# Kernel tuning notes

Hardware: AMD Instinct MI355X
Metric: run time of the kernel (lower is better)

Reference implementation:

```python
import jax, jax.numpy as jnp
import numpy as np

IN_C, H1, H2, FC1, NCLS = 16, 32, 64, 128, 10
N_NODES, N_EDGES = 20000, 100000


def _glorot(key, shape):
    fan_in, fan_out = shape[0], shape[-1]
    s = jnp.sqrt(6.0 / (fan_in + fan_out))
    return jax.random.uniform(key, shape, jnp.float32, -s, s)


def setup_inputs() -> dict:
    key = jax.random.key(0)
    ks = jax.random.split(key, 20)
    x = jax.random.normal(ks[0], (N_NODES, IN_C), jnp.float32)
    edge_index = jax.random.randint(ks[1], (2, N_EDGES), 0, N_NODES, jnp.int64)
    edge_attr = jax.random.uniform(ks[2], (N_EDGES, 1), jnp.float32)
    return {
        "x": x,
        "edge_index": edge_index,
        "edge_attr": edge_attr,
        # conv1 edge-MLP: 1 -> 25 -> IN_C*H1
        "w1a": _glorot(ks[3], (1, 25)), "b1a": jnp.zeros((25,), jnp.float32),
        "w1b": _glorot(ks[4], (25, IN_C * H1)), "b1b": jnp.zeros((IN_C * H1,), jnp.float32),
        "wr1": _glorot(ks[5], (IN_C, H1)), "bias1": jnp.zeros((H1,), jnp.float32),
        # conv2 edge-MLP: 1 -> 25 -> H1*H2 (=2048)
        "w2a": _glorot(ks[6], (1, 25)), "b2a": jnp.zeros((25,), jnp.float32),
        "w2b": _glorot(ks[7], (25, H1 * H2)), "b2b": jnp.zeros((H1 * H2,), jnp.float32),
        "wr2": _glorot(ks[8], (H1, H2)), "bias2": jnp.zeros((H2,), jnp.float32),
        # trailing FCs
        "fc1_w": _glorot(ks[9], (H2, FC1)), "fc1_b": jnp.zeros((FC1,), jnp.float32),
        "fc2_w": _glorot(ks[10], (FC1, NCLS)), "fc2_b": jnp.zeros((NCLS,), jnp.float32),
    }


def _nnconv(x, src, tgt, edge_attr, wa, ba, wb, bb, wroot, bias, in_c, out_c):
    # per-edge MLP-generated weight matrix [E, in_c, out_c]
    h = jax.nn.relu(edge_attr @ wa + ba) @ wb + bb
    W = h.reshape(-1, in_c, out_c)
    # gather source feats, per-edge matmul, scatter-max to targets
    msg = jnp.einsum("ei,eio->eo", x[src], W)  # [E, out_c]
    agg = jax.ops.segment_max(msg, tgt, num_segments=x.shape[0])
    agg = jnp.where(jnp.isfinite(agg), agg, 0.0)  # nodes with no in-edges -> 0 (PyG behavior)
    return agg + x @ wroot + bias


def reference(x, edge_index, edge_attr,
              w1a, b1a, w1b, b1b, wr1, bias1,
              w2a, b2a, w2b, b2b, wr2, bias2,
              fc1_w, fc1_b, fc2_w, fc2_b):
    src, tgt = edge_index[0], edge_index[1]
    h = jax.nn.elu(_nnconv(x, src, tgt, edge_attr, w1a, b1a, w1b, b1b, wr1, bias1, IN_C, H1))
    h = jax.nn.elu(_nnconv(h, src, tgt, edge_attr, w2a, b2a, w2b, b2b, wr2, bias2, H1, H2))
    h = jax.nn.elu(h @ fc1_w + fc1_b)
    h = h @ fc2_w + fc2_b
    return jax.nn.log_softmax(h, axis=1)
```

## Files before the change

### kernel.cpp

```cpp
#include <hip/hip_runtime.h>
#include <float.h>
#include <math.h>


#define NCONST 25
#define CH1 32
#define CH2 16
#define PACK_MASK 0x1FFFF

typedef float vf16 __attribute__((ext_vector_type(16)));
typedef float vf32 __attribute__((ext_vector_type(32)));

__device__ __forceinline__ void atomicMaxFloat(float* addr, float val) {
    if (val >= 0.f) atomicMax((int*)addr, __float_as_int(val));
    else            atomicMin((unsigned int*)addr, __float_as_uint(val));
}
__device__ __forceinline__ float readlane_f(float v, int l) {
    return __int_as_float(__builtin_amdgcn_readlane(__float_as_int(v), l));
}

__global__ void fill_kernel(float* agg, int nAgg, int* ords, int nOrd, int* hist, int nH) {
    int i = blockIdx.x * blockDim.x + threadIdx.x;
    int stride = gridDim.x * blockDim.x;
    int total = nAgg + nOrd + nH;
    for (; i < total; i += stride) {
        if (i < nAgg) agg[i] = -FLT_MAX;
        else if (i < nAgg + nOrd) ords[i - nAgg] = -1;
        else hist[i - nAgg - nOrd] = 0;
    }
}

__global__ void assign_hist_kernel(const float* __restrict__ ea,
                                   const float* __restrict__ w1a, const float* __restrict__ b1a,
                                   const float* __restrict__ w2a, const float* __restrict__ b2a,
                                   int E, int* __restrict__ segpack, int* __restrict__ hist) {
    __shared__ float t1[NCONST], t2[NCONST];
    __shared__ int lh[64];
    int tid = threadIdx.x;
    if (tid < NCONST) {
        float w = w1a[tid]; t1[tid] = (w != 0.f) ? (-b1a[tid] / w) : INFINITY;
        float v = w2a[tid]; t2[tid] = (v != 0.f) ? (-b2a[tid] / v) : INFINITY;
    }
    if (tid < 64) lh[tid] = 0;
    __syncthreads();
    int e = blockIdx.x * blockDim.x + tid;
    bool valid = e < E;
    if (valid) {
        float a = ea[e];
        int j1 = 0, j2 = 0;
        for (int k = 0; k < NCONST; ++k) { j1 += (t1[k] < a); j2 += (t2[k] < a); }
        segpack[e] = j1 | (j2 << 8);
        atomicAdd(&lh[j1], 1); atomicAdd(&lh[32 + j2], 1);
    }
    __syncthreads();
    if (tid < 64 && lh[tid]) atomicAdd(&hist[tid], lh[tid]);
}

__global__ void scanpad_kernel(const int* __restrict__ hist, int* __restrict__ cur) {
    __shared__ int h[64];
    int tid = threadIdx.x;
    h[tid] = hist[tid];
    __syncthreads();
    if (tid == 0) {
        int off = 0;
        for (int j = 0; j < 26; ++j) { cur[j] = off; off += ((h[j] + CH1 - 1) / CH1) * CH1; }
    } else if (tid == 1) {
        int off = 0;
        for (int j = 0; j < 26; ++j) { cur[32 + j] = off; off += ((h[32 + j] + CH2 - 1) / CH2) * CH2; }
    }
}

__global__ void scatter_kernel(const int* __restrict__ segpack, int E, int* __restrict__ cur,
                               int* __restrict__ order1, int* __restrict__ order2) {
    __shared__ int lh[64], lb[64];
    int tid = threadIdx.x;
    if (tid < 64) lh[tid] = 0;
    __syncthreads();
    int e = blockIdx.x * blockDim.x + tid;
    bool valid = e < E;
    int j1 = 0, j2 = 0, r1 = 0, r2 = 0;
    if (valid) {
        int p = segpack[e]; j1 = p & 0xFF; j2 = p >> 8;
        r1 = atomicAdd(&lh[j1], 1); r2 = atomicAdd(&lh[32 + j2], 1);
    }
    __syncthreads();
    if (tid < 64 && lh[tid]) lb[tid] = atomicAdd(&cur[tid], lh[tid]);
    __syncthreads();
    if (valid) {
        order1[lb[j1] + r1] = (j1 << 17) | e;
        order2[lb[32 + j2] + r2] = (j2 << 17) | e;
    }
}

__global__ void build_uv_fused(const float* w1a, const float* b1a, const float* w1b, const float* b1b,
                               const float* w2a, const float* b2a, const float* w2b, const float* b2b,
                               float* U1, float* V1, float* U2, float* V2) {
    __shared__ float swa[NCONST], sba[NCONST], st[NCONST];
    __shared__ int sr[NCONST];
    __shared__ unsigned msk_sh;
    int seg = blockIdx.y;
    int bx = blockIdx.x;
    int conv = (bx < 2) ? 0 : 1;
    const float* wa = conv ? w2a : w1a;
    const float* ba = conv ? b2a : b1a;
    int tid = threadIdx.x;
    if (tid < NCONST) {
        float w = wa[tid], b = ba[tid];
        swa[tid] = w; sba[tid] = b;
        st[tid] = (w != 0.f) ? (-b / w) : INFINITY;
    }
    __syncthreads();
    if (tid < NCONST) {
        int rk = 0;
        for (int l = 0; l < NCONST; ++l) rk += (st[l] < st[tid]) ? 1 : 0;
        sr[tid] = rk;
    }
    __syncthreads();
    if (tid == 0) {
        unsigned m = 0;
        for (int k = 0; k < NCONST; ++k) {
            float w = swa[k];
            bool act = (w > 0.f) ? (seg > sr[k])
                     : (w < 0.f) ? (seg <= sr[k])
                                 : (sba[k] > 0.f);
            if (act) m |= (1u << k);
        }
        msk_sh = m;
    }
    __syncthreads();
    unsigned msk = msk_sh;
    if (conv == 0) {
        int idx = bx * 256 + tid;
        float u = 0.f, v = 0.f;
        for (int k = 0; k < NCONST; ++k)
            if (msk & (1u << k)) { float w = w1b[k * 512 + idx]; u = fmaf(swa[k], w, u); v = fmaf(sba[k], w, v); }
        v += b1b[idx];
        U1[seg * 512 + idx] = u; V1[seg * 512 + idx] = v;
    } else {
        int idx = (bx - 2) * 256 + tid;
        float u = 0.f, v = 0.f;
        for (int k = 0; k < NCONST; ++k)
            if (msk & (1u << k)) { float w = w2b[k * 2048 + idx]; u = fmaf(swa[k], w, u); v = fmaf(sba[k], w, v); }
        v += b2b[idx];
        U2[seg * 2048 + idx] = u; V2[seg * 2048 + idx] = v;
    }
}

__global__ void __launch_bounds__(256, 4)
edge1_kernel(const float* __restrict__ xin, const int* __restrict__ src,
             const int* __restrict__ tgt, const float* __restrict__ ea,
             const int* __restrict__ order, int cap,
             const float* __restrict__ U, const float* __restrict__ V,
             float* __restrict__ agg) {
    int wid = (blockIdx.x * blockDim.x + threadIdx.x) >> 6;
    int lane = threadIdx.x & 63;
    int base = wid * CH1;
    if (base >= cap) return;
    int pk = order[base + (lane & (CH1 - 1))];
    int p0 = __builtin_amdgcn_readfirstlane(pk);
    if (p0 < 0) return;
    int seg = p0 >> 17;
    int ev = (pk < 0) ? 0 : (pk & PACK_MASK);
    int sv = src[ev], tv = tgt[ev];
    float av = ea[ev];
    int half = lane >> 5, c = lane & 31;
    vf16 Ur, Vr;
    {
        const float* Us = U + seg * 512 + c;
        const float* Vs = V + seg * 512 + c;
#pragma unroll
        for (int i = 0; i < 16; ++i) { Ur[i] = Us[i * 32]; Vr[i] = Vs[i * 32]; }
    }
#pragma unroll
    for (int t = 0; t < CH1; t += 2) {
        int pA = __builtin_amdgcn_readlane(pk, t);
        int pB = __builtin_amdgcn_readlane(pk, t + 1);
        int sA = __builtin_amdgcn_readlane(sv, t);
        int sB = __builtin_amdgcn_readlane(sv, t + 1);
        int tA = __builtin_amdgcn_readlane(tv, t);
        int tB = __builtin_amdgcn_readlane(tv, t + 1);
        float aA = readlane_f(av, t);
        float aB = readlane_f(av, t + 1);
        const float* xA = xin + sA * 16;
        const float* xB = xin + sB * 16;
        float ah = half ? aB : aA;
        int   th = half ? tB : tA;
        int   ph = half ? pB : pA;
        float acc = 0.f;
#pragma unroll
        for (int i = 0; i < 16; ++i) {
            float xi = half ? xB[i] : xA[i];
            acc = fmaf(xi, fmaf(ah, Ur[i], Vr[i]), acc);
        }
        if (ph >= 0) atomicMaxFloat(&agg[th * 32 + c], acc);
    }
}

__global__ void __launch_bounds__(256, 2)
edge2_kernel(const float* __restrict__ xin, const int* __restrict__ src,
             const int* __restrict__ tgt, const float* __restrict__ ea,
             const int* __restrict__ order, int cap,
             const float* __restrict__ U, const float* __restrict__ V,
             float* __restrict__ agg) {
    int wid = (blockIdx.x * blockDim.x + threadIdx.x) >> 6;
    int lane = threadIdx.x & 63;
    int base = wid * CH2;
    if (base >= cap) return;
    int pk = order[base + (lane & (CH2 - 1))];
    int p0 = __builtin_amdgcn_readfirstlane(pk);
    if (p0 < 0) return;
    int seg = p0 >> 17;
    int ev = (pk < 0) ? 0 : (pk & PACK_MASK);
    int sv = src[ev], tv = tgt[ev];
    float av = ea[ev];
    vf32 Ur, Vr;
    {
        const float* Us = U + seg * 2048 + lane;
        const float* Vs = V + seg * 2048 + lane;
#pragma unroll
        for (int i = 0; i < 32; ++i) { Ur[i] = Us[i * 64]; Vr[i] = Vs[i * 64]; }
    }
#pragma unroll
    for (int t = 0; t < CH2; t += 2) {
        int pA = __builtin_amdgcn_readlane(pk, t);
        int pB = __builtin_amdgcn_readlane(pk, t + 1);
        int sA = __builtin_amdgcn_readlane(sv, t);
        int sB = __builtin_amdgcn_readlane(sv, t + 1);
        int tA = __builtin_amdgcn_readlane(tv, t);
        int tB = __builtin_amdgcn_readlane(tv, t + 1);
        float aA = readlane_f(av, t);
        float aB = readlane_f(av, t + 1);
        const float* xA = xin + sA * 32;
        const float* xB = xin + sB * 32;
        float accA = 0.f, accB = 0.f;
#pragma unroll
        for (int i = 0; i < 32; ++i) {
            accA = fmaf(xA[i], fmaf(aA, Ur[i], Vr[i]), accA);
            accB = fmaf(xB[i], fmaf(aB, Ur[i], Vr[i]), accB);
        }
        if (pA >= 0) atomicMaxFloat(&agg[tA * 64 + lane], accA);
        if (pB >= 0) atomicMaxFloat(&agg[tB * 64 + lane], accB);
    }
}

__global__ void node1_kernel(const float* __restrict__ xin, const float* __restrict__ agg,
                             const float* __restrict__ wroot, const float* __restrict__ bias,
                             float* __restrict__ out, int N) {
    int idx = blockIdx.x * blockDim.x + threadIdx.x;
    if (idx >= N * 32) return;
    int n = idx >> 5, c = idx & 31;
    float v = agg[idx];
    if (v == -FLT_MAX) v = 0.f;
    float acc = v + bias[c];
#pragma unroll
    for (int i = 0; i < 16; ++i) acc = fmaf(xin[n * 16 + i], wroot[i * 32 + c], acc);
    out[idx] = acc > 0.f ? acc : expm1f(acc);
}

#define TAIL_NPB 8
__global__ void __launch_bounds__(256)
tail_kernel(const float* __restrict__ h1, const float* __restrict__ agg2,
            const float* __restrict__ wr2, const float* __restrict__ bias2,
            const float* __restrict__ fc1w, const float* __restrict__ fc1b,
            const float* __restrict__ fc2w, const float* __restrict__ fc2b,
            float* __restrict__ out) {
    __shared__ __align__(16) float wr2s[2048];
    __shared__ __align__(16) float f1ws[8192];
    __shared__ __align__(16) float f2ws[1280];
    __shared__ float b2s[64], f1bs[128], f2bs[16];
    __shared__ __align__(16) float h2sh[4][64];
    __shared__ __align__(16) float h3sh[4][128];
    int tid = threadIdx.x;
    for (int i = tid; i < 2048; i += 256) wr2s[i] = wr2[i];
    for (int i = tid; i < 8192; i += 256) f1ws[i] = fc1w[i];
    for (int i = tid; i < 1280; i += 256) f2ws[i] = fc2w[i];
    if (tid < 64)  b2s[tid]  = bias2[tid];
    if (tid < 128) f1bs[tid] = fc1b[tid];
    if (tid < 10)  f2bs[tid] = fc2b[tid];
    __syncthreads();
    int w = tid >> 6, lane = tid & 63;
    int n0 = blockIdx.x * TAIL_NPB + w * (TAIL_NPB / 4);
    for (int it = 0; it < TAIL_NPB / 4; ++it) {
        int n = n0 + it;
        float v = agg2[n * 64 + lane];
        if (v == -FLT_MAX) v = 0.f;
        float acc = v + b2s[lane];
        const float* xr = h1 + n * 32;
#pragma unroll
        for (int i = 0; i < 32; ++i) acc = fmaf(xr[i], wr2s[i * 64 + lane], acc);
        h2sh[w][lane] = acc > 0.f ? acc : expm1f(acc);
        const float4* h2v = (const float4*)h2sh[w];
#pragma unroll
        for (int r = 0; r < 2; ++r) {
            int o = lane + r * 64;
            float a1 = f1bs[o];
#pragma unroll
            for (int q = 0; q < 16; ++q) {
                float4 hv = h2v[q];
                a1 = fmaf(hv.x, f1ws[(q * 4 + 0) * 128 + o], a1);
                a1 = fmaf(hv.y, f1ws[(q * 4 + 1) * 128 + o], a1);
                a1 = fmaf(hv.z, f1ws[(q * 4 + 2) * 128 + o], a1);
                a1 = fmaf(hv.w, f1ws[(q * 4 + 3) * 128 + o], a1);
            }
            h3sh[w][o] = a1 > 0.f ? a1 : expm1f(a1);
        }
        float logit = -FLT_MAX;
        const float4* h3v = (const float4*)h3sh[w];
        if (lane < 10) {
            float a2 = f2bs[lane];
#pragma unroll
            for (int q = 0; q < 32; ++q) {
                float4 hv = h3v[q];
                a2 = fmaf(hv.x, f2ws[(q * 4 + 0) * 10 + lane], a2);
                a2 = fmaf(hv.y, f2ws[(q * 4 + 1) * 10 + lane], a2);
                a2 = fmaf(hv.z, f2ws[(q * 4 + 2) * 10 + lane], a2);
                a2 = fmaf(hv.w, f2ws[(q * 4 + 3) * 10 + lane], a2);
            }
            logit = a2;
        }
        float mx = -FLT_MAX;
#pragma unroll
        for (int i = 0; i < 10; ++i) mx = fmaxf(mx, __shfl(logit, i, 64));
        float s = 0.f;
#pragma unroll
        for (int i = 0; i < 10; ++i) s += expf(__shfl(logit, i, 64) - mx);
        if (lane < 10) out[n * 10 + lane] = logit - mx - logf(s);
    }
}

extern "C" void kernel_launch(void* const* d_in, const int* in_sizes, int n_in,
                              void* d_out, int out_size, void* d_ws, size_t ws_size,
                              hipStream_t stream) {
    const float* x     = (const float*)d_in[0];
    const int*   eidx  = (const int*)d_in[1];
    const float* ea    = (const float*)d_in[2];
    const float* w1a   = (const float*)d_in[3];
    const float* b1a   = (const float*)d_in[4];
    const float* w1b   = (const float*)d_in[5];
    const float* b1b   = (const float*)d_in[6];
    const float* wr1   = (const float*)d_in[7];
    const float* bias1 = (const float*)d_in[8];
    const float* w2a   = (const float*)d_in[9];
    const float* b2a   = (const float*)d_in[10];
    const float* w2b   = (const float*)d_in[11];
    const float* b2b   = (const float*)d_in[12];
    const float* wr2   = (const float*)d_in[13];
    const float* bias2 = (const float*)d_in[14];
    const float* fc1w  = (const float*)d_in[15];
    const float* fc1b  = (const float*)d_in[16];
    const float* fc2w  = (const float*)d_in[17];
    const float* fc2b  = (const float*)d_in[18];

    const int N = in_sizes[0] / 16;
    const int E = in_sizes[2];
    const int* src = eidx;
    const int* tgt = eidx + E;

    const int cap1 = ((E + 26 * (CH1 - 1)) + CH1 - 1) / CH1 * CH1;
    const int cap2 = ((E + 26 * (CH2 - 1)) + CH2 - 1) / CH2 * CH2;

    float* ws = (float*)d_ws;
    size_t off = 0;
    int*      hist = (int*)(ws + off);      off += 64;
    int*      cur  = (int*)(ws + off);      off += 64;
    int*      segp = (int*)(ws + off);      off += E;
    int*      ord1 = (int*)(ws + off);      off += cap1;
    int*      ord2 = (int*)(ws + off);      off += cap2;
    float*    U1   = ws + off;              off += 26 * 512;
    float*    V1   = ws + off;              off += 26 * 512;
    float*    U2   = ws + off;              off += 26 * 2048;
    float*    V2   = ws + off;              off += 26 * 2048;
    float*    AGG1 = ws + off;              off += (size_t)N * 32;
    float*    AGG2 = ws + off;              off += (size_t)N * 64;
    float*    H1b  = ws + off;              off += (size_t)N * 32;

    fill_kernel<<<512, 256, 0, stream>>>(AGG1, N * 96, ord1, cap1 + cap2, hist, 64);
    assign_hist_kernel<<<(E + 255) / 256, 256, 0, stream>>>(ea, w1a, b1a, w2a, b2a, E, segp, hist);
    scanpad_kernel<<<1, 64, 0, stream>>>(hist, cur);
    scatter_kernel<<<(E + 255) / 256, 256, 0, stream>>>(segp, E, cur, ord1, ord2);
    build_uv_fused<<<dim3(10, 26), 256, 0, stream>>>(w1a, b1a, w1b, b1b, w2a, b2a, w2b, b2b,
                                                     U1, V1, U2, V2);
    {
        int waves = cap1 / CH1;
        edge1_kernel<<<(waves + 3) / 4, 256, 0, stream>>>(x, src, tgt, ea, ord1, cap1, U1, V1, AGG1);
    }
    node1_kernel<<<(N * 32 + 255) / 256, 256, 0, stream>>>(x, AGG1, wr1, bias1, H1b, N);
    {
        int waves = cap2 / CH2;
        edge2_kernel<<<(waves + 3) / 4, 256, 0, stream>>>(H1b, src, tgt, ea, ord2, cap2, U2, V2, AGG2);
    }
    tail_kernel<<<N / TAIL_NPB, 256, 0, stream>>>(H1b, AGG2, wr2, bias2, fc1w, fc1b, fc2w, fc2b,
                                                  (float*)d_out);
}
```

Measured before the change: 234.2 us.

## Restructure tail kernel to one thread per node with register-held activations

The tail kernel now maps one node to each thread instead of one node per wavefront. Each thread keeps its 64-wide and 128-wide activations in registers, and all lanes read the same weight addresses, so weight loads become uniform. Shared memory now holds only transposed h2 values, and the per-block weight staging into LDS is removed. ELU and log-softmax switch to fast exp/log intrinsics. The costs are much higher register pressure, only 79 blocks of work on the device, and slightly lower accuracy in exp.

```diff
diff --git a/kernel.cpp b/kernel.cpp
--- a/kernel.cpp
+++ b/kernel.cpp
@@ -17,6 +17,9 @@
 }
 __device__ __forceinline__ float readlane_f(float v, int l) {
     return __int_as_float(__builtin_amdgcn_readlane(__float_as_int(v), l));
+}
+__device__ __forceinline__ float elu_fast(float x) {
+    return x > 0.f ? x : (__expf(x) - 1.f);
 }
 
 __global__ void fill_kernel(float* agg, int nAgg, int* ords, int nOrd, int* hist, int nH) {
@@ -257,74 +260,76 @@
     out[idx] = acc > 0.f ? acc : expm1f(acc);
 }
 
-#define TAIL_NPB 8
-__global__ void __launch_bounds__(256)
+__global__ void __launch_bounds__(256, 2)
 tail_kernel(const float* __restrict__ h1, const float* __restrict__ agg2,
             const float* __restrict__ wr2, const float* __restrict__ bias2,
             const float* __restrict__ fc1w, const float* __restrict__ fc1b,
             const float* __restrict__ fc2w, const float* __restrict__ fc2b,
-            float* __restrict__ out) {
-    __shared__ __align__(16) float wr2s[2048];
-    __shared__ __align__(16) float f1ws[8192];
-    __shared__ __align__(16) float f2ws[1280];
-    __shared__ float b2s[64], f1bs[128], f2bs[16];
-    __shared__ __align__(16) float h2sh[4][64];
-    __shared__ __align__(16) float h3sh[4][128];
-    int tid = threadIdx.x;
-    for (int i = tid; i < 2048; i += 256) wr2s[i] = wr2[i];
-    for (int i = tid; i < 8192; i += 256) f1ws[i] = fc1w[i];
-    for (int i = tid; i < 1280; i += 256) f2ws[i] = fc2w[i];
-    if (tid < 64)  b2s[tid]  = bias2[tid];
-    if (tid < 128) f1bs[tid] = fc1b[tid];
-    if (tid < 10)  f2bs[tid] = fc2b[tid];
-    __syncthreads();
-    int w = tid >> 6, lane = tid & 63;
-    int n0 = blockIdx.x * TAIL_NPB + w * (TAIL_NPB / 4);
-    for (int it = 0; it < TAIL_NPB / 4; ++it) {
-        int n = n0 + it;
-        float v = agg2[n * 64 + lane];
-        if (v == -FLT_MAX) v = 0.f;
-        float acc = v + b2s[lane];
-        const float* xr = h1 + n * 32;
-#pragma unroll
-        for (int i = 0; i < 32; ++i) acc = fmaf(xr[i], wr2s[i * 64 + lane], acc);
-        h2sh[w][lane] = acc > 0.f ? acc : expm1f(acc);
-        const float4* h2v = (const float4*)h2sh[w];
-#pragma unroll
-        for (int r = 0; r < 2; ++r) {
-            int o = lane + r * 64;
-            float a1 = f1bs[o];
-#pragma unroll
-            for (int q = 0; q < 16; ++q) {
-                float4 hv = h2v[q];
-                a1 = fmaf(hv.x, f1ws[(q * 4 + 0) * 128 + o], a1);
-                a1 = fmaf(hv.y, f1ws[(q * 4 + 1) * 128 + o], a1);
-                a1 = fmaf(hv.z, f1ws[(q * 4 + 2) * 128 + o], a1);
-                a1 = fmaf(hv.w, f1ws[(q * 4 + 3) * 128 + o], a1);
-            }
-            h3sh[w][o] = a1 > 0.f ? a1 : expm1f(a1);
-        }
-        float logit = -FLT_MAX;
-        const float4* h3v = (const float4*)h3sh[w];
-        if (lane < 10) {
-            float a2 = f2bs[lane];
-#pragma unroll
-            for (int q = 0; q < 32; ++q) {
-                float4 hv = h3v[q];
-                a2 = fmaf(hv.x, f2ws[(q * 4 + 0) * 10 + lane], a2);
-                a2 = fmaf(hv.y, f2ws[(q * 4 + 1) * 10 + lane], a2);
-                a2 = fmaf(hv.z, f2ws[(q * 4 + 2) * 10 + lane], a2);
-                a2 = fmaf(hv.w, f2ws[(q * 4 + 3) * 10 + lane], a2);
-            }
-            logit = a2;
-        }
-        float mx = -FLT_MAX;
-#pragma unroll
-        for (int i = 0; i < 10; ++i) mx = fmaxf(mx, __shfl(logit, i, 64));
-        float s = 0.f;
-#pragma unroll
-        for (int i = 0; i < 10; ++i) s += expf(__shfl(logit, i, 64) - mx);
-        if (lane < 10) out[n * 10 + lane] = logit - mx - logf(s);
+            float* __restrict__ out, int N) {
+    __shared__ float h2sh[64 * 256];
+    int tid = threadIdx.x;
+    int n = blockIdx.x * 256 + tid;
+    bool valid = n < N;
+    int nc = valid ? n : N - 1;
+
+    float h2[64];
+    {
+        const float4* a2v = (const float4*)(agg2 + (size_t)nc * 64);
+#pragma unroll
+        for (int q = 0; q < 16; ++q) {
+            float4 t = a2v[q];
+            h2[q*4+0] = (t.x == -FLT_MAX ? 0.f : t.x) + bias2[q*4+0];
+            h2[q*4+1] = (t.y == -FLT_MAX ? 0.f : t.y) + bias2[q*4+1];
+            h2[q*4+2] = (t.z == -FLT_MAX ? 0.f : t.z) + bias2[q*4+2];
+            h2[q*4+3] = (t.w == -FLT_MAX ? 0.f : t.w) + bias2[q*4+3];
+        }
+    }
+    const float* h1r = h1 + (size_t)nc * 32;
+    for (int i = 0; i < 32; ++i) {
+        float xi = h1r[i];
+        const float* wrow = wr2 + i * 64;
+#pragma unroll
+        for (int o = 0; o < 64; ++o) h2[o] = fmaf(xi, wrow[o], h2[o]);
+    }
+#pragma unroll
+    for (int o = 0; o < 64; ++o) {
+        float v = elu_fast(h2[o]);
+        h2sh[o * 256 + tid] = v;
+    }
+
+    float oacc[10];
+#pragma unroll
+    for (int c = 0; c < 10; ++c) oacc[c] = fc2b[c];
+#pragma unroll
+    for (int half = 0; half < 2; ++half) {
+        float h3[64];
+#pragma unroll
+        for (int o = 0; o < 64; ++o) h3[o] = fc1b[half * 64 + o];
+        for (int i = 0; i < 64; ++i) {
+            float hi = h2sh[i * 256 + tid];
+            const float* wrow = fc1w + i * 128 + half * 64;
+#pragma unroll
+            for (int o = 0; o < 64; ++o) h3[o] = fmaf(hi, wrow[o], h3[o]);
+        }
+#pragma unroll
+        for (int o = 0; o < 64; ++o) {
+            float v = elu_fast(h3[o]);
+            const float* w2r = fc2w + (half * 64 + o) * 10;
+#pragma unroll
+            for (int c = 0; c < 10; ++c) oacc[c] = fmaf(v, w2r[c], oacc[c]);
+        }
+    }
+
+    float mx = oacc[0];
+#pragma unroll
+    for (int c = 1; c < 10; ++c) mx = fmaxf(mx, oacc[c]);
+    float s = 0.f;
+#pragma unroll
+    for (int c = 0; c < 10; ++c) s += __expf(oacc[c] - mx);
+    float lse = mx + __logf(s);
+    if (valid) {
+#pragma unroll
+        for (int c = 0; c < 10; ++c) out[(size_t)n * 10 + c] = oacc[c] - lse;
     }
 }
 
@@ -389,6 +394,6 @@
         int waves = cap2 / CH2;
         edge2_kernel<<<(waves + 3) / 4, 256, 0, stream>>>(H1b, src, tgt, ea, ord2, cap2, U2, V2, AGG2);
     }
-    tail_kernel<<<N / TAIL_NPB, 256, 0, stream>>>(H1b, AGG2, wr2, bias2, fc1w, fc1b, fc2w, fc2b,
-                                                  (float*)d_out);
-}
+    tail_kernel<<<(N + 255) / 256, 256, 0, stream>>>(H1b, AGG2, wr2, bias2, fc1w, fc1b, fc2w, fc2b,
+                                                     (float*)d_out, N);
+}
```

New measurement: 290.2 us. 23.9% more time.
